# Performance work log

Hardware: AMD Instinct MI355X
Metric: run time of the kernel (lower is better)

Reference implementation:

```python
import jax, jax.numpy as jnp
import numpy as np
import math

B, T, D = 2, 2048, 1024
H = 16
HD = D // H
DFF = 4096
EPS = 1e-5


def setup_inputs() -> dict:
    key = jax.random.key(0)
    ks = jax.random.split(key, 11)
    s = 0.02
    return {
        "x": jax.random.normal(ks[0], (B, T, D), dtype=jnp.float32),
        "scale1": jnp.ones((D,), jnp.float32),
        "scale2": jnp.ones((D,), jnp.float32),
        "Wqkv": jax.random.normal(ks[1], (D, 3 * D), jnp.float32) * s,
        "bqkv": jnp.zeros((3 * D,), jnp.float32),
        "Wo": jax.random.normal(ks[2], (D, D), jnp.float32) * s,
        "bo": jnp.zeros((D,), jnp.float32),
        "W1": jax.random.normal(ks[3], (D, DFF), jnp.float32) * s,
        "b1": jnp.zeros((DFF,), jnp.float32),
        "W2": jax.random.normal(ks[4], (DFF, D), jnp.float32) * s,
        "b2": jnp.zeros((D,), jnp.float32),
    }


def rmsnorm(x, scale):
    # Faithful to source: norm = ||x||/sqrt(d); out = scale * x / (norm + eps)
    d = x.shape[-1]
    norm = jnp.linalg.norm(x, axis=-1, keepdims=True) * (1.0 / math.sqrt(d))
    return scale * x / (norm + EPS)


def attention(x, Wqkv, bqkv, Wo, bo):
    b, t, c = x.shape
    qkv = x @ Wqkv + bqkv                       # [B,T,3D]
    qkv = qkv.reshape(b, t, 3, H, HD)
    q, k, v = qkv[:, :, 0], qkv[:, :, 1], qkv[:, :, 2]   # [B,T,H,HD]
    scores = jnp.einsum("bqhd,bkhd->bhqk", q, k) / math.sqrt(HD)
    w = jax.nn.softmax(scores, axis=-1)
    out = jnp.einsum("bhqk,bkhd->bqhd", w, v).reshape(b, t, c)
    return out @ Wo + bo


def reference(x, scale1, scale2, Wqkv, bqkv, Wo, bo, W1, b1, W2, b2):
    x = x + attention(rmsnorm(x, scale1), Wqkv, bqkv, Wo, bo)
    h = rmsnorm(x, scale2)
    ff = (jax.nn.gelu(h @ W1 + b1, approximate=False)) @ W2 + b2
    return x + ff
```

## Files before the change

### kernel.cpp

```cpp
#include <hip/hip_runtime.h>
#include <hip/hip_bf16.h>
#include <math.h>

typedef unsigned short u16;
typedef __bf16 bf16x8 __attribute__((ext_vector_type(8)));
typedef float f32x4 __attribute__((ext_vector_type(4)));
typedef unsigned int u32x2 __attribute__((ext_vector_type(2)));

#define B_   2
#define T_   2048
#define D_   1024
#define H_   16
#define HD_  64
#define DFF_ 4096
#define M_TOK (B_*T_)

__device__ __forceinline__ u16 f2bf(float f){
  unsigned u = __float_as_uint(f);
  u += 0x7fff + ((u>>16)&1);
  return (u16)(u>>16);
}

__device__ __forceinline__ void gl2lds16(const void* g, void* l){
  __builtin_amdgcn_global_load_lds((const __attribute__((address_space(1))) void*)g,
                                   (__attribute__((address_space(3))) void*)l, 16, 0, 0);
}

__device__ __forceinline__ unsigned lds_u32(const void* p){
  return (unsigned)(uintptr_t)(const __attribute__((address_space(3))) void*)p;
}

__device__ __forceinline__ u32x2 tr_read(unsigned addr){
  u32x2 d;
  asm volatile("ds_read_b64_tr_b16 %0, %1" : "=v"(d) : "v"(addr));
  return d;
}
__device__ __forceinline__ u32x2 tr_read512(unsigned addr){
  u32x2 d;
  asm volatile("ds_read_b64_tr_b16 %0, %1 offset:512" : "=v"(d) : "v"(addr));
  return d;
}
__device__ __forceinline__ bf16x8 pack8(u32x2 a, u32x2 b){
  union { u32x2 u[2]; bf16x8 v; } x; x.u[0]=a; x.u[1]=b; return x.v;
}
__device__ __forceinline__ unsigned cvt_pk_bf16(float a, float b){
  unsigned r;
  asm("v_cvt_pk_bf16_f32 %0, %1, %2" : "=v"(r) : "v"(a), "v"(b));
  return r;
}

__device__ __forceinline__ void block_barrier(){
  asm volatile("" ::: "memory");
  __builtin_amdgcn_s_barrier();
  __builtin_amdgcn_sched_barrier(0);
  asm volatile("" ::: "memory");
}

__global__ __launch_bounds__(256) void k_transpose_bf16(const float* __restrict__ in,
                                                        u16* __restrict__ out, int K, int N){
  __shared__ float t[32][33];
  int bx = blockIdx.x*32, by = blockIdx.y*32;
  int tx = threadIdx.x, ty = threadIdx.y;
  #pragma unroll
  for(int i=ty;i<32;i+=8) t[i][tx] = in[(size_t)(by+i)*N + bx + tx];
  __syncthreads();
  #pragma unroll
  for(int i=ty;i<32;i+=8) out[(size_t)(bx+i)*K + by + tx] = f2bf(t[tx][i]);
}

__global__ __launch_bounds__(256) void k_rmsnorm_bf16(const float* __restrict__ x,
                                                      const float* __restrict__ scale,
                                                      u16* __restrict__ out){
  int row = blockIdx.x;
  int tid = threadIdx.x;
  int lane = tid&63, wave = tid>>6;
  const float4* xr = (const float4*)(x + (size_t)row*D_);
  float4 v = xr[tid];
  float ss = v.x*v.x + v.y*v.y + v.z*v.z + v.w*v.w;
  #pragma unroll
  for(int o=1;o<64;o<<=1) ss += __shfl_xor(ss, o);
  __shared__ float red[4];
  if(lane==0) red[wave]=ss;
  __syncthreads();
  float tot = red[0]+red[1]+red[2]+red[3];
  float inv = 1.0f/(sqrtf(tot*(1.0f/D_)) + 1e-5f);
  const float4* sr = (const float4*)scale;
  float4 s4 = sr[tid];
  u16* o4 = out + (size_t)row*D_ + tid*4;
  o4[0]=f2bf(v.x*s4.x*inv); o4[1]=f2bf(v.y*s4.y*inv);
  o4[2]=f2bf(v.z*s4.z*inv); o4[3]=f2bf(v.w*s4.w*inv);
}

template<int EPI>
__global__ __launch_bounds__(512,2) void k_gemm256(const u16* __restrict__ A, const u16* __restrict__ Bt,
                                                   const float* __restrict__ bias,
                                                   void* __restrict__ Cout, int M, int N, int K){
  __shared__ u16 LDS[4][16384];
  const int tid = threadIdx.x;
  const int lane = tid&63, wave = tid>>6;
  const int lo = lane&15, hi = lane>>4;
  const int wm = wave>>2, wn = wave&3;
  const int row0 = blockIdx.x*256, col0 = blockIdx.y*256;
  f32x4 acc[8][4];
  #pragma unroll
  for(int m=0;m<8;m++)
    #pragma unroll
    for(int n=0;n<4;n++) acc[m][n] = (f32x4){0.f,0.f,0.f,0.f};
  const u16* Ag = A + (size_t)row0*K;
  const u16* Bg = Bt + (size_t)col0*K;
  const int NT = K>>5;

  const int cc0 = tid, cc1 = tid+512;
  const size_t s0 = (size_t)(cc0>>2)*K + (size_t)((((cc0&3)^((cc0>>3)&3)))<<3);
  const size_t s1 = (size_t)(cc1>>2)*K + (size_t)((((cc1&3)^((cc1>>3)&3)))<<3);

  #define STAGE_A(t) { const u16* Ab = Ag + (size_t)(t)*32; char* d = (char*)LDS[(t)&3]; \
    gl2lds16(Ab + s0, d + cc0*16); gl2lds16(Ab + s1, d + cc1*16); }
  #define STAGE_B(t) { const u16* Bb = Bg + (size_t)(t)*32; char* d = (char*)LDS[(t)&3] + 16384; \
    gl2lds16(Bb + s0, d + cc0*16); gl2lds16(Bb + s1, d + cc1*16); }

  STAGE_A(0); STAGE_B(0); STAGE_A(1); STAGE_B(1); STAGE_A(2); STAGE_B(2);

  const unsigned slot = (unsigned)((hi ^ ((lo>>1)&3))<<4);
  for(int t=0;t<NT;t++){
    if(t<NT-2)       { asm volatile("s_waitcnt vmcnt(8)" ::: "memory"); }
    else if(t==NT-2) { asm volatile("s_waitcnt vmcnt(4)" ::: "memory"); }
    else             { asm volatile("s_waitcnt vmcnt(0)" ::: "memory"); }
    block_barrier();
    const char* bufp = (const char*)LDS[t&3];
    const char* ap = bufp + (wm*128 + lo)*64 + slot;
    const char* bp = bufp + 16384 + (wn*64 + lo)*64 + slot;

    if(t+3<NT) STAGE_A(t+3);
    __builtin_amdgcn_sched_barrier(0);
    bf16x8 a0[4], b[4];
    #pragma unroll
    for(int m=0;m<4;m++) a0[m] = *(const bf16x8*)(ap + m*1024);
    #pragma unroll
    for(int n=0;n<4;n++) b[n]  = *(const bf16x8*)(bp + n*1024);
    __builtin_amdgcn_s_setprio(1);
    #pragma unroll
    for(int m=0;m<4;m++)
      #pragma unroll
      for(int n=0;n<4;n++)
        acc[m][n] = __builtin_amdgcn_mfma_f32_16x16x32_bf16(a0[m], b[n], acc[m][n], 0,0,0);
    __builtin_amdgcn_s_setprio(0);

    if(t+3<NT) STAGE_B(t+3);
    __builtin_amdgcn_sched_barrier(0);
    bf16x8 a1[4];
    #pragma unroll
    for(int m=0;m<4;m++) a1[m] = *(const bf16x8*)(ap + 4096 + m*1024);
    __builtin_amdgcn_s_setprio(1);
    #pragma unroll
    for(int m=0;m<4;m++)
      #pragma unroll
      for(int n=0;n<4;n++)
        acc[m+4][n] = __builtin_amdgcn_mfma_f32_16x16x32_bf16(a1[m], b[n], acc[m+4][n], 0,0,0);
    __builtin_amdgcn_s_setprio(0);
  }
  #undef STAGE_A
  #undef STAGE_B

  #pragma unroll
  for(int m=0;m<8;m++){
    #pragma unroll
    for(int n=0;n<4;n++){
      #pragma unroll
      for(int r=0;r<4;r++){
        int row = row0 + wm*128 + m*16 + hi*4 + r;
        int col = col0 + wn*64 + n*16 + lo;
        float v = acc[m][n][r] + bias[col];
        if constexpr(EPI==2){
          v = 0.5f*v*(1.0f + erff(v*0.70710678118f));
        }
        ((u16*)Cout)[(size_t)row*N + col] = f2bf(v);
      }
    }
  }
}

template<int EPI>
__global__ __launch_bounds__(256) void k_gemm(const u16* __restrict__ A, const u16* __restrict__ Bt,
                                              const float* __restrict__ bias, const float* __restrict__ res,
                                              void* __restrict__ Cout, int M, int N, int K){
  __shared__ u16 As[128*32];
  __shared__ u16 Bs[128*32];
  int tid = threadIdx.x;
  int lane = tid&63, wave = tid>>6;
  int lo = lane&15, hi = lane>>4;
  int wr = wave>>1, wc = wave&1;
  int row0 = blockIdx.x*128, col0 = blockIdx.y*128;
  f32x4 acc[4][4];
  #pragma unroll
  for(int m=0;m<4;m++)
    #pragma unroll
    for(int n=0;n<4;n++) acc[m][n] = (f32x4){0.f,0.f,0.f,0.f};
  const u16* Ag = A + (size_t)row0*K;
  const u16* Bg = Bt + (size_t)col0*K;
  const unsigned sw = (unsigned)((hi^((lo>>1)&3))*16);
  for(int k0=0;k0<K;k0+=32){
    __syncthreads();
    #pragma unroll
    for(int c=tid;c<512;c+=256){
      gl2lds16(Ag + (size_t)(c>>2)*K + k0 + (size_t)(((c&3)^((c>>3)&3))<<3), (char*)As + c*16);
      gl2lds16(Bg + (size_t)(c>>2)*K + k0 + (size_t)(((c&3)^((c>>3)&3))<<3), (char*)Bs + c*16);
    }
    __syncthreads();
    const char* ab = (const char*)As + (wr*64+lo)*64;
    const char* bb = (const char*)Bs + (wc*64+lo)*64;
    bf16x8 a[4], b[4];
    #pragma unroll
    for(int m=0;m<4;m++) a[m] = *(const bf16x8*)(ab + m*1024 + sw);
    #pragma unroll
    for(int n=0;n<4;n++) b[n] = *(const bf16x8*)(bb + n*1024 + sw);
    #pragma unroll
    for(int m=0;m<4;m++)
      #pragma unroll
      for(int n=0;n<4;n++)
        acc[m][n] = __builtin_amdgcn_mfma_f32_16x16x32_bf16(a[m], b[n], acc[m][n], 0,0,0);
  }
  #pragma unroll
  for(int m=0;m<4;m++){
    #pragma unroll
    for(int n=0;n<4;n++){
      #pragma unroll
      for(int r=0;r<4;r++){
        int row = row0 + wr*64 + m*16 + hi*4 + r;
        int col = col0 + wc*64 + n*16 + lo;
        float v = acc[m][n][r] + bias[col];
        if constexpr(EPI==1){
          ((float*)Cout)[(size_t)row*N + col] = v + res[(size_t)row*N + col];
        } else if constexpr(EPI==2){
          v = 0.5f*v*(1.0f + erff(v*0.70710678118f));
          ((u16*)Cout)[(size_t)row*N + col] = f2bf(v);
        } else {
          ((u16*)Cout)[(size_t)row*N + col] = f2bf(v);
        }
      }
    }
  }
}

__global__ __launch_bounds__(256) void k_gemm_pk(const u16* __restrict__ A, const u16* __restrict__ Bt,
                                                 float* __restrict__ P, int M, int N, int K){
  __shared__ u16 As[128*32];
  __shared__ u16 Bs[128*32];
  int tid = threadIdx.x;
  int lane = tid&63, wave = tid>>6;
  int lo = lane&15, hi = lane>>4;
  int wr = wave>>1, wc = wave&1;
  int row0 = blockIdx.x*128, col0 = blockIdx.y*128;
  int kc = blockIdx.z;
  int klen = K/2, kbeg = kc*klen;
  f32x4 acc[4][4];
  #pragma unroll
  for(int m=0;m<4;m++)
    #pragma unroll
    for(int n=0;n<4;n++) acc[m][n] = (f32x4){0.f,0.f,0.f,0.f};
  const u16* Ag = A + (size_t)row0*K + kbeg;
  const u16* Bg = Bt + (size_t)col0*K + kbeg;
  const unsigned sw = (unsigned)((hi^((lo>>1)&3))*16);
  for(int k0=0;k0<klen;k0+=32){
    __syncthreads();
    #pragma unroll
    for(int c=tid;c<512;c+=256){
      gl2lds16(Ag + (size_t)(c>>2)*K + k0 + (size_t)(((c&3)^((c>>3)&3))<<3), (char*)As + c*16);
      gl2lds16(Bg + (size_t)(c>>2)*K + k0 + (size_t)(((c&3)^((c>>3)&3))<<3), (char*)Bs + c*16);
    }
    __syncthreads();
    const char* ab = (const char*)As + (wr*64+lo)*64;
    const char* bb = (const char*)Bs + (wc*64+lo)*64;
    bf16x8 a[4], b[4];
    #pragma unroll
    for(int m=0;m<4;m++) a[m] = *(const bf16x8*)(ab + m*1024 + sw);
    #pragma unroll
    for(int n=0;n<4;n++) b[n] = *(const bf16x8*)(bb + n*1024 + sw);
    #pragma unroll
    for(int m=0;m<4;m++)
      #pragma unroll
      for(int n=0;n<4;n++)
        acc[m][n] = __builtin_amdgcn_mfma_f32_16x16x32_bf16(a[m], b[n], acc[m][n], 0,0,0);
  }
  float* Pk = P + (size_t)kc*M*N;
  #pragma unroll
  for(int m=0;m<4;m++)
    #pragma unroll
    for(int n=0;n<4;n++)
      #pragma unroll
      for(int r=0;r<4;r++){
        int row = row0 + wr*64 + m*16 + hi*4 + r;
        int col = col0 + wc*64 + n*16 + lo;
        Pk[(size_t)row*N + col] = acc[m][n][r];
      }
}

__global__ __launch_bounds__(256) void k_ff2_reduce(const float* __restrict__ P,
                                                    const float* __restrict__ bias,
                                                    const float* __restrict__ res,
                                                    float* __restrict__ out){
  const size_t total4 = (size_t)M_TOK*D_/4;
  const float4* p0 = (const float4*)P;
  const float4* p1 = (const float4*)(P + (size_t)M_TOK*D_);
  const float4* rr = (const float4*)res;
  const float4* bb = (const float4*)bias;
  float4* oo = (float4*)out;
  for(size_t i = (size_t)blockIdx.x*256 + threadIdx.x; i < total4; i += (size_t)gridDim.x*256){
    float4 a = p0[i], b = p1[i], r = rr[i], c = bb[i & (D_/4 - 1)];
    float4 o;
    o.x = (a.x+b.x)+(c.x+r.x);
    o.y = (a.y+b.y)+(c.y+r.y);
    o.z = (a.z+b.z)+(c.z+r.z);
    o.w = (a.w+b.w)+(c.w+r.w);
    oo[i] = o;
  }
}

__global__ __launch_bounds__(256,4) void k_attn(const u16* __restrict__ qkv, u16* __restrict__ O){
  __shared__ alignas(16) u16 Ks[2][4096];
  __shared__ alignas(16) u16 Vs[2][4096];
  __shared__ alignas(16) u16 Ps[4][1024];
  const int qt = blockIdx.x, h = blockIdx.y, b = blockIdx.z;
  const int tid = threadIdx.x, lane = tid&63, wave = tid>>6;
  const int lo = lane&15, hi = lane>>4, l7 = lane&7;
  const u16* qkvB = qkv + (size_t)b*T_*3072;
  const int hoff = h*64;
  const float C2 = 0.18033688f;

  const int q0 = qt*64 + wave*16;
  const u16* qp = qkvB + (size_t)(q0+lo)*3072 + hoff + hi*8;
  bf16x8 aq0 = *(const bf16x8*)qp;
  bf16x8 aq1 = *(const bf16x8*)(qp+32);

  size_t sK[2], sV[2];
  {
    int cc[2] = {tid, tid+256};
    #pragma unroll
    for(int i=0;i<2;i++){
      int c = cc[i];
      sK[i] = (size_t)(c>>3)*3072 + 1024 + hoff + (((c&7)^((c>>3)&7))<<3);
      int kv = ((c>>5)<<2) + ((c>>1)&3);
      int d0 = (((c&31)>>3)<<4) | ((c&1)<<3);
      sV[i] = (size_t)kv*3072 + 2048 + hoff + d0;
    }
  }
  const unsigned kb0 = (unsigned)lo*128 + (unsigned)((hi^l7))*16;
  const unsigned kb1 = (unsigned)lo*128 + (unsigned)(((hi|4)^l7))*16;
  const unsigned vtr = (unsigned)hi*1024 + (unsigned)lo*2;
  const unsigned swzQ = (unsigned)(lo&7)<<4;

  f32x4 oac[4];
  #pragma unroll
  for(int n=0;n<4;n++) oac[n] = (f32x4){0.f,0.f,0.f,0.f};
  float mrow = -1e30f;
  float lsum = 0.f;

  {
    char* kd = (char*)Ks[0]; char* vd = (char*)Vs[0];
    gl2lds16(qkvB + sK[0], kd + tid*16);
    gl2lds16(qkvB + sK[1], kd + tid*16 + 4096);
    gl2lds16(qkvB + sV[0], vd + tid*16);
    gl2lds16(qkvB + sV[1], vd + tid*16 + 4096);
  }
  int buf = 0;
  for(int t=0;t<T_/64;t++){
    __syncthreads();
    if(t < T_/64-1){
      size_t koff = (size_t)(t+1)*64*3072;
      char* kd = (char*)Ks[buf^1]; char* vd = (char*)Vs[buf^1];
      gl2lds16(qkvB + koff + sK[0], kd + tid*16);
      gl2lds16(qkvB + koff + sK[1], kd + tid*16 + 4096);
      gl2lds16(qkvB + koff + sV[0], vd + tid*16);
      gl2lds16(qkvB + koff + sV[1], vd + tid*16 + 4096);
    }
    const char* K_ = (const char*)Ks[buf];
    u16* P_ = Ps[wave];

    f32x4 s[4];
    __builtin_amdgcn_s_setprio(1);
    #pragma unroll
    for(int n=0;n<4;n++){
      bf16x8 k0f = *(const bf16x8*)(K_ + n*2048 + kb0);
      bf16x8 k1f = *(const bf16x8*)(K_ + n*2048 + kb1);
      f32x4 z = (f32x4){0.f,0.f,0.f,0.f};
      z = __builtin_amdgcn_mfma_f32_16x16x32_bf16(k0f, aq0, z, 0,0,0);
      z = __builtin_amdgcn_mfma_f32_16x16x32_bf16(k1f, aq1, z, 0,0,0);
      s[n] = z;
    }
    __builtin_amdgcn_s_setprio(0);

    float mx = s[0][0];
    #pragma unroll
    for(int n=0;n<4;n++)
      #pragma unroll
      for(int r=0;r<4;r++) mx = fmaxf(mx, s[n][r]);

    if(!__all(mx <= mrow + 64.0f)){
      float mm = fmaxf(mx, __shfl_xor(mx,16));
      mm = fmaxf(mm, __shfl_xor(mm,32));
      float nm = fmaxf(mrow, mm);
      float alpha = exp2f((mrow - nm)*C2);
      mrow = nm;
      lsum *= alpha;
      float ar[4];
      #pragma unroll
      for(int r=0;r<4;r++) ar[r] = __shfl(alpha, hi*4 + r);
      #pragma unroll
      for(int n=0;n<4;n++)
        #pragma unroll
        for(int r=0;r<4;r++) oac[n][r] *= ar[r];
    }

    const float nmC2 = -mrow*C2;
    #pragma unroll
    for(int n=0;n<4;n++){
      float p0v = exp2f(fmaf(s[n][0], C2, nmC2));
      float p1v = exp2f(fmaf(s[n][1], C2, nmC2));
      float p2v = exp2f(fmaf(s[n][2], C2, nmC2));
      float p3v = exp2f(fmaf(s[n][3], C2, nmC2));
      lsum += (p0v+p1v)+(p2v+p3v);
      u32x2 pw;
      pw[0] = cvt_pk_bf16(p0v, p1v);
      pw[1] = cvt_pk_bf16(p2v, p3v);
      *(u32x2*)((char*)P_ + (unsigned)lo*128 + (((unsigned)(n*32 + hi*8)) ^ swzQ)) = pw;
    }

    const unsigned vsb = lds_u32(Vs[buf]);
    #pragma unroll
    for(int kk=0;kk<2;kk++){
      bf16x8 ap = *(const bf16x8*)((const char*)P_ + (kk==0 ? kb0 : kb1));
      u32x2 t0[4], t1[4];
      #pragma unroll
      for(int n=0;n<4;n++){
        unsigned a = vsb + vtr + (unsigned)kk*4096 + (unsigned)n*128;
        t0[n] = tr_read(a);
        t1[n] = tr_read512(a);
      }
      asm volatile("s_waitcnt lgkmcnt(0)" ::: "memory");
      __builtin_amdgcn_sched_barrier(0);
      __builtin_amdgcn_s_setprio(1);
      #pragma unroll
      for(int n=0;n<4;n++){
        bf16x8 bv = pack8(t0[n], t1[n]);
        oac[n] = __builtin_amdgcn_mfma_f32_16x16x32_bf16(ap, bv, oac[n], 0,0,0);
      }
      __builtin_amdgcn_s_setprio(0);
    }
    buf ^= 1;
  }

  lsum += __shfl_xor(lsum, 16);
  lsum += __shfl_xor(lsum, 32);
  float linv = 1.0f/lsum;
  float lr[4];
  #pragma unroll
  for(int r=0;r<4;r++) lr[r] = __shfl(linv, hi*4 + r);
  size_t obase = ((size_t)b*T_ + q0)*D_ + hoff;
  #pragma unroll
  for(int n=0;n<4;n++)
    #pragma unroll
    for(int r=0;r<4;r++)
      O[obase + (size_t)(hi*4+r)*D_ + n*16 + lo] = f2bf(oac[n][r]*lr[r]);
}

extern "C" void kernel_launch(void* const* d_in, const int* in_sizes, int n_in,
                              void* d_out, int out_size, void* d_ws, size_t ws_size,
                              hipStream_t stream){
  (void)in_sizes; (void)n_in; (void)out_size; (void)ws_size;
  const float* x      = (const float*)d_in[0];
  const float* scale1 = (const float*)d_in[1];
  const float* scale2 = (const float*)d_in[2];
  const float* Wqkv   = (const float*)d_in[3];
  const float* bqkv   = (const float*)d_in[4];
  const float* Wo     = (const float*)d_in[5];
  const float* bo     = (const float*)d_in[6];
  const float* W1     = (const float*)d_in[7];
  const float* b1     = (const float*)d_in[8];
  const float* W2     = (const float*)d_in[9];
  const float* b2     = (const float*)d_in[10];
  float* out = (float*)d_out;

  char* w = (char*)d_ws;
  u16* xn1   = (u16*)w;  w += (size_t)M_TOK*D_*2;
  u16* qkvb  = (u16*)w;  w += (size_t)M_TOK*3*D_*2;
  u16* Obuf  = (u16*)w;  w += (size_t)M_TOK*D_*2;
  float* x2  = (float*)w; w += (size_t)M_TOK*D_*4;
  u16* xn2   = (u16*)w;  w += (size_t)M_TOK*D_*2;
  u16* h1    = (u16*)w;  w += (size_t)M_TOK*DFF_*2;
  u16* Wqkvt = (u16*)w;  w += (size_t)3*D_*D_*2;
  u16* Wot   = (u16*)w;  w += (size_t)D_*D_*2;
  u16* W1t   = (u16*)w;  w += (size_t)D_*DFF_*2;
  u16* W2t   = (u16*)w;  w += (size_t)DFF_*D_*2;
  float* pk  = (float*)d_ws;

  dim3 tb(32,8);
  k_transpose_bf16<<<dim3(3*D_/32, D_/32), tb, 0, stream>>>(Wqkv, Wqkvt, D_, 3*D_);
  k_transpose_bf16<<<dim3(D_/32,   D_/32), tb, 0, stream>>>(Wo,   Wot,   D_, D_);
  k_transpose_bf16<<<dim3(DFF_/32, D_/32), tb, 0, stream>>>(W1,   W1t,   D_, DFF_);
  k_transpose_bf16<<<dim3(D_/32, DFF_/32), tb, 0, stream>>>(W2,   W2t,   DFF_, D_);

  k_rmsnorm_bf16<<<M_TOK, 256, 0, stream>>>(x, scale1, xn1);
  k_gemm256<0><<<dim3(M_TOK/256, 3*D_/256), 512, 0, stream>>>(xn1, Wqkvt, bqkv, qkvb, M_TOK, 3*D_, D_);
  k_attn<<<dim3(T_/64, H_, B_), 256, 0, stream>>>(qkvb, Obuf);
  k_gemm<1><<<dim3(M_TOK/128, D_/128), 256, 0, stream>>>(Obuf, Wot, bo, x, x2, M_TOK, D_, D_);
  k_rmsnorm_bf16<<<M_TOK, 256, 0, stream>>>(x2, scale2, xn2);
  k_gemm256<2><<<dim3(M_TOK/256, DFF_/256), 512, 0, stream>>>(xn2, W1t, b1, h1, M_TOK, DFF_, D_);
  k_gemm_pk<<<dim3(M_TOK/128, D_/128, 2), 256, 0, stream>>>(h1, W2t, pk, M_TOK, D_, DFF_);
  k_ff2_reduce<<<2048, 256, 0, stream>>>(pk, b2, x2, out);
}
```

Baseline: 272.7 us.

## Process two query subtiles per wave in attention to reuse K/V fragments

Each attention wave now handles 32 query rows (two 16-row groups) instead of 16, so the block covers 128 queries and the grid halves. K fragments and transposed V reads from LDS are shared across both groups, which halves LDS traffic and global K/V loads per query. The cost is more registers (launch bounds drop to 2 blocks per SIMD), a larger P buffer, and fewer blocks (512), which may lower occupancy and latency hiding.

```diff
diff --git a/kernel.cpp b/kernel.cpp
--- a/kernel.cpp
+++ b/kernel.cpp
@@ -316,10 +316,10 @@
   }
 }
 
-__global__ __launch_bounds__(256,4) void k_attn(const u16* __restrict__ qkv, u16* __restrict__ O){
+__global__ __launch_bounds__(256,2) void k_attn(const u16* __restrict__ qkv, u16* __restrict__ O){
   __shared__ alignas(16) u16 Ks[2][4096];
   __shared__ alignas(16) u16 Vs[2][4096];
-  __shared__ alignas(16) u16 Ps[4][1024];
+  __shared__ alignas(16) u16 Ps[4][2048];
   const int qt = blockIdx.x, h = blockIdx.y, b = blockIdx.z;
   const int tid = threadIdx.x, lane = tid&63, wave = tid>>6;
   const int lo = lane&15, hi = lane>>4, l7 = lane&7;
@@ -327,10 +327,16 @@
   const int hoff = h*64;
   const float C2 = 0.18033688f;
 
-  const int q0 = qt*64 + wave*16;
-  const u16* qp = qkvB + (size_t)(q0+lo)*3072 + hoff + hi*8;
-  bf16x8 aq0 = *(const bf16x8*)qp;
-  bf16x8 aq1 = *(const bf16x8*)(qp+32);
+  const int q0 = qt*128 + wave*32;
+  bf16x8 aq[2][2];
+  {
+    const u16* qp = qkvB + (size_t)(q0+lo)*3072 + hoff + hi*8;
+    aq[0][0] = *(const bf16x8*)qp;
+    aq[0][1] = *(const bf16x8*)(qp+32);
+    const u16* qp1 = qp + 16*3072;
+    aq[1][0] = *(const bf16x8*)qp1;
+    aq[1][1] = *(const bf16x8*)(qp1+32);
+  }
 
   size_t sK[2], sV[2];
   {
@@ -349,11 +355,13 @@
   const unsigned vtr = (unsigned)hi*1024 + (unsigned)lo*2;
   const unsigned swzQ = (unsigned)(lo&7)<<4;
 
-  f32x4 oac[4];
-  #pragma unroll
-  for(int n=0;n<4;n++) oac[n] = (f32x4){0.f,0.f,0.f,0.f};
-  float mrow = -1e30f;
-  float lsum = 0.f;
+  f32x4 oac[2][4];
+  #pragma unroll
+  for(int g=0;g<2;g++)
+    #pragma unroll
+    for(int n=0;n<4;n++) oac[g][n] = (f32x4){0.f,0.f,0.f,0.f};
+  float mrow[2] = {-1e30f,-1e30f};
+  float lsum[2] = {0.f,0.f};
 
   {
     char* kd = (char*)Ks[0]; char* vd = (char*)Vs[0];
@@ -374,61 +382,77 @@
       gl2lds16(qkvB + koff + sV[1], vd + tid*16 + 4096);
     }
     const char* K_ = (const char*)Ks[buf];
-    u16* P_ = Ps[wave];
-
-    f32x4 s[4];
+    char* P_ = (char*)Ps[wave];
+
+    f32x4 s[2][4];
     __builtin_amdgcn_s_setprio(1);
     #pragma unroll
     for(int n=0;n<4;n++){
       bf16x8 k0f = *(const bf16x8*)(K_ + n*2048 + kb0);
       bf16x8 k1f = *(const bf16x8*)(K_ + n*2048 + kb1);
-      f32x4 z = (f32x4){0.f,0.f,0.f,0.f};
-      z = __builtin_amdgcn_mfma_f32_16x16x32_bf16(k0f, aq0, z, 0,0,0);
-      z = __builtin_amdgcn_mfma_f32_16x16x32_bf16(k1f, aq1, z, 0,0,0);
-      s[n] = z;
+      #pragma unroll
+      for(int g=0;g<2;g++){
+        f32x4 z = (f32x4){0.f,0.f,0.f,0.f};
+        z = __builtin_amdgcn_mfma_f32_16x16x32_bf16(k0f, aq[g][0], z, 0,0,0);
+        z = __builtin_amdgcn_mfma_f32_16x16x32_bf16(k1f, aq[g][1], z, 0,0,0);
+        s[g][n] = z;
+      }
     }
     __builtin_amdgcn_s_setprio(0);
 
-    float mx = s[0][0];
-    #pragma unroll
-    for(int n=0;n<4;n++)
-      #pragma unroll
-      for(int r=0;r<4;r++) mx = fmaxf(mx, s[n][r]);
-
-    if(!__all(mx <= mrow + 64.0f)){
-      float mm = fmaxf(mx, __shfl_xor(mx,16));
-      mm = fmaxf(mm, __shfl_xor(mm,32));
-      float nm = fmaxf(mrow, mm);
-      float alpha = exp2f((mrow - nm)*C2);
-      mrow = nm;
-      lsum *= alpha;
-      float ar[4];
-      #pragma unroll
-      for(int r=0;r<4;r++) ar[r] = __shfl(alpha, hi*4 + r);
+    float mx[2];
+    #pragma unroll
+    for(int g=0;g<2;g++){
+      float m0 = s[g][0][0];
       #pragma unroll
       for(int n=0;n<4;n++)
         #pragma unroll
-        for(int r=0;r<4;r++) oac[n][r] *= ar[r];
-    }
-
-    const float nmC2 = -mrow*C2;
-    #pragma unroll
-    for(int n=0;n<4;n++){
-      float p0v = exp2f(fmaf(s[n][0], C2, nmC2));
-      float p1v = exp2f(fmaf(s[n][1], C2, nmC2));
-      float p2v = exp2f(fmaf(s[n][2], C2, nmC2));
-      float p3v = exp2f(fmaf(s[n][3], C2, nmC2));
-      lsum += (p0v+p1v)+(p2v+p3v);
-      u32x2 pw;
-      pw[0] = cvt_pk_bf16(p0v, p1v);
-      pw[1] = cvt_pk_bf16(p2v, p3v);
-      *(u32x2*)((char*)P_ + (unsigned)lo*128 + (((unsigned)(n*32 + hi*8)) ^ swzQ)) = pw;
+        for(int r=0;r<4;r++) m0 = fmaxf(m0, s[g][n][r]);
+      mx[g] = m0;
+    }
+
+    if(!__all(mx[0] <= mrow[0]+64.0f && mx[1] <= mrow[1]+64.0f)){
+      #pragma unroll
+      for(int g=0;g<2;g++){
+        float mm = fmaxf(mx[g], __shfl_xor(mx[g],16));
+        mm = fmaxf(mm, __shfl_xor(mm,32));
+        float nm = fmaxf(mrow[g], mm);
+        float alpha = exp2f((mrow[g]-nm)*C2);
+        mrow[g] = nm;
+        lsum[g] *= alpha;
+        float ar[4];
+        #pragma unroll
+        for(int r=0;r<4;r++) ar[r] = __shfl(alpha, hi*4 + r);
+        #pragma unroll
+        for(int n=0;n<4;n++)
+          #pragma unroll
+          for(int r=0;r<4;r++) oac[g][n][r] *= ar[r];
+      }
+    }
+
+    #pragma unroll
+    for(int g=0;g<2;g++){
+      const float nmC2 = -mrow[g]*C2;
+      #pragma unroll
+      for(int n=0;n<4;n++){
+        float p0v = exp2f(fmaf(s[g][n][0], C2, nmC2));
+        float p1v = exp2f(fmaf(s[g][n][1], C2, nmC2));
+        float p2v = exp2f(fmaf(s[g][n][2], C2, nmC2));
+        float p3v = exp2f(fmaf(s[g][n][3], C2, nmC2));
+        lsum[g] += (p0v+p1v)+(p2v+p3v);
+        u32x2 pw;
+        pw[0] = cvt_pk_bf16(p0v, p1v);
+        pw[1] = cvt_pk_bf16(p2v, p3v);
+        *(u32x2*)(P_ + g*2048 + (unsigned)lo*128 + (((unsigned)(n*32 + hi*8)) ^ swzQ)) = pw;
+      }
     }
 
     const unsigned vsb = lds_u32(Vs[buf]);
     #pragma unroll
     for(int kk=0;kk<2;kk++){
-      bf16x8 ap = *(const bf16x8*)((const char*)P_ + (kk==0 ? kb0 : kb1));
+      const unsigned kb = (kk==0 ? kb0 : kb1);
+      bf16x8 ap0 = *(const bf16x8*)(P_ + kb);
+      bf16x8 ap1 = *(const bf16x8*)(P_ + 2048 + kb);
       u32x2 t0[4], t1[4];
       #pragma unroll
       for(int n=0;n<4;n++){
@@ -442,25 +466,30 @@
       #pragma unroll
       for(int n=0;n<4;n++){
         bf16x8 bv = pack8(t0[n], t1[n]);
-        oac[n] = __builtin_amdgcn_mfma_f32_16x16x32_bf16(ap, bv, oac[n], 0,0,0);
+        oac[0][n] = __builtin_amdgcn_mfma_f32_16x16x32_bf16(ap0, bv, oac[0][n], 0,0,0);
+        oac[1][n] = __builtin_amdgcn_mfma_f32_16x16x32_bf16(ap1, bv, oac[1][n], 0,0,0);
       }
       __builtin_amdgcn_s_setprio(0);
     }
     buf ^= 1;
   }
 
-  lsum += __shfl_xor(lsum, 16);
-  lsum += __shfl_xor(lsum, 32);
-  float linv = 1.0f/lsum;
-  float lr[4];
-  #pragma unroll
-  for(int r=0;r<4;r++) lr[r] = __shfl(linv, hi*4 + r);
   size_t obase = ((size_t)b*T_ + q0)*D_ + hoff;
   #pragma unroll
-  for(int n=0;n<4;n++)
-    #pragma unroll
-    for(int r=0;r<4;r++)
-      O[obase + (size_t)(hi*4+r)*D_ + n*16 + lo] = f2bf(oac[n][r]*lr[r]);
+  for(int g=0;g<2;g++){
+    float ls = lsum[g];
+    ls += __shfl_xor(ls, 16);
+    ls += __shfl_xor(ls, 32);
+    float linv = 1.0f/ls;
+    float lr[4];
+    #pragma unroll
+    for(int r=0;r<4;r++) lr[r] = __shfl(linv, hi*4 + r);
+    #pragma unroll
+    for(int n=0;n<4;n++)
+      #pragma unroll
+      for(int r=0;r<4;r++)
+        O[obase + (size_t)(g*16 + hi*4+r)*D_ + n*16 + lo] = f2bf(oac[g][n][r]*lr[r]);
+  }
 }
 
 extern "C" void kernel_launch(void* const* d_in, const int* in_sizes, int n_in,
@@ -501,7 +530,7 @@
 
   k_rmsnorm_bf16<<<M_TOK, 256, 0, stream>>>(x, scale1, xn1);
   k_gemm256<0><<<dim3(M_TOK/256, 3*D_/256), 512, 0, stream>>>(xn1, Wqkvt, bqkv, qkvb, M_TOK, 3*D_, D_);
-  k_attn<<<dim3(T_/64, H_, B_), 256, 0, stream>>>(qkvb, Obuf);
+  k_attn<<<dim3(T_/128, H_, B_), 256, 0, stream>>>(qkvb, Obuf);
   k_gemm<1><<<dim3(M_TOK/128, D_/128), 256, 0, stream>>>(Obuf, Wot, bo, x, x2, M_TOK, D_, D_);
   k_rmsnorm_bf16<<<M_TOK, 256, 0, stream>>>(x2, scale2, xn2);
   k_gemm256<2><<<dim3(M_TOK/256, DFF_/256), 512, 0, stream>>>(xn2, W1t, b1, h1, M_TOK, DFF_, D_);
```

Measured after the change: 274.5 us. Within noise of the previous version (+0.6%).
